# Optimization experiments

Measured on AMD Instinct MI355X. Metric: run time of the kernel, lower is better.

The kernel has to match this reference:

```python
import jax, jax.numpy as jnp
import numpy as np

N, D, E, L = 50000, 128, 800000, 3


def setup_inputs() -> dict:
    key = jax.random.key(0)
    ks = jax.random.split(key, 4)
    scale = 1.0 / np.sqrt(D)
    x = jax.random.normal(ks[0], (N, D), dtype=jnp.float32)
    edge_index = jax.random.randint(ks[1], (2, E), 0, N, dtype=jnp.int64)
    W1 = jax.random.normal(ks[2], (L, D, D), dtype=jnp.float32) * scale
    W2 = jax.random.normal(ks[3], (L, D, D), dtype=jnp.float32) * scale
    b1 = jnp.zeros((L, D), dtype=jnp.float32)
    b2 = jnp.zeros((L, D), dtype=jnp.float32)
    return {"x": x, "edge_index": edge_index, "W1": W1, "b1": b1, "W2": W2, "b2": b2}


def reference(x, edge_index, W1, b1, W2, b2):
    # GIN: for each conv, agg_i = (1+eps)*x_i + sum_{(j->i)} x_j  (eps=0),
    # then h = nn(agg) with nn = Linear->ReLU->Linear, then outer ReLU.
    src = edge_index[0]
    dst = edge_index[1]
    n = x.shape[0]
    for l in range(W1.shape[0]):
        agg = x + jax.ops.segment_sum(x[src], dst, num_segments=n)  # [N, D]
        h = jnp.maximum(agg @ W1[l] + b1[l], 0.0)                   # inner ReLU
        x = jnp.maximum(h @ W2[l] + b2[l], 0.0)                     # outer ReLU
    return x
```

## Files before the change

kernel.cpp:

```cpp
#include <hip/hip_runtime.h>
#include <cstdint>


constexpr int N = 50000;
constexpr int D = 128;
constexpr int E = 800000;
constexpr int L = 3;
constexpr int WROW = 136;
constexpr int PSH = 9;
constexpr int PN = 1 << PSH;
constexpr int K = (N + PN - 1) >> PSH;
constexpr int ABLK = 2048;
constexpr int NAB = (E + ABLK - 1) / ABLK;

typedef _Float16 f16;
typedef _Float16 f16x8 __attribute__((ext_vector_type(8)));
typedef float f32x4 __attribute__((ext_vector_type(4)));

__device__ __forceinline__ bool ei_is64(const int* ei) {
  return (ei[1] == 0) && (ei[3] == 0) && (ei[5] == 0);
}
__device__ __forceinline__ int ei_src(const int* ei, int e, bool is64) {
  return is64 ? ei[2 * (size_t)e] : ei[e];
}
__device__ __forceinline__ int ei_dst(const int* ei, int e, bool is64) {
  return is64 ? ei[2 * ((size_t)E + e)] : ei[(size_t)E + e];
}

__global__ __launch_bounds__(256) void k_init(const float* __restrict__ x0,
                                              const int* __restrict__ ei,
                                              const float* __restrict__ W1,
                                              const float* __restrict__ W2,
                                              f16* __restrict__ Wt,
                                              f16* __restrict__ xh,
                                              int2* __restrict__ srcdst,
                                              int* __restrict__ gcnt) {
  __shared__ int hist[K];
  const int bid = blockIdx.x;
  if (bid < 384) {
    int i = bid * 256 + threadIdx.x;
    int m = i >> 14;
    int c = (i >> 7) & 127;
    int k = i & 127;
    const float* src = (m < L) ? (W1 + (size_t)m * D * D)
                               : (W2 + (size_t)(m - L) * D * D);
    Wt[i] = (f16)src[(size_t)k * D + c];
  } else if (bid < 384 + 3125) {
    int i = (bid - 384) * 256 + threadIdx.x;
    float4 v0 = *(const float4*)(x0 + (size_t)i * 8);
    float4 v1 = *(const float4*)(x0 + (size_t)i * 8 + 4);
    f16x8 o = {(f16)v0.x, (f16)v0.y, (f16)v0.z, (f16)v0.w,
               (f16)v1.x, (f16)v1.y, (f16)v1.z, (f16)v1.w};
    *(f16x8*)(xh + (size_t)i * 8) = o;
  } else {
    const int b = bid - (384 + 3125);
    for (int i = threadIdx.x; i < K; i += 256) hist[i] = 0;
    __syncthreads();
    const int base = b * ABLK;
    const int nHere = min(ABLK, E - base);
    bool is64 = ei_is64(ei);
#pragma unroll
    for (int r = 0; r < ABLK / 256; ++r) {
      int idx = r * 256 + threadIdx.x;
      if (idx < nHere) {
        int e = base + idx;
        int s = ei_src(ei, e, is64);
        int d = ei_dst(ei, e, is64);
        srcdst[e] = make_int2(s, d);
        atomicAdd(&hist[d >> PSH], 1);
      }
    }
    __syncthreads();
    for (int i = threadIdx.x; i < K; i += 256) gcnt[i * NAB + b] = hist[i];
  }
}

__global__ __launch_bounds__(256) void k_gbase(const int* __restrict__ gcnt,
                                               int* __restrict__ gbase,
                                               int* __restrict__ psize) {
  __shared__ int s[256];
  __shared__ int carry;
  const int p = blockIdx.x;
  const int tid = threadIdx.x;
  if (tid == 0) carry = 0;
  __syncthreads();
  for (int chunk = 0; chunk < 2; ++chunk) {
    int i = chunk * 256 + tid;
    int v = (i < NAB) ? gcnt[p * NAB + i] : 0;
    s[tid] = v;
    __syncthreads();
#pragma unroll
    for (int o = 1; o < 256; o <<= 1) {
      int t = (tid >= o) ? s[tid - o] : 0;
      __syncthreads();
      s[tid] += t;
      __syncthreads();
    }
    int excl = s[tid] - v + carry;
    if (i < NAB) gbase[p * NAB + i] = excl;
    __syncthreads();
    if (tid == 255) carry = carry + s[255];
    __syncthreads();
  }
  if (tid == 0) psize[p] = carry;
}

__global__ __launch_bounds__(256) void k_pscan(const int* __restrict__ psize,
                                               int* __restrict__ pbase,
                                               int* __restrict__ off) {
  __shared__ int s[256];
  const int tid = threadIdx.x;
  int v = (tid < K) ? psize[tid] : 0;
  s[tid] = v;
  __syncthreads();
#pragma unroll
  for (int o = 1; o < 256; o <<= 1) {
    int t = (tid >= o) ? s[tid - o] : 0;
    __syncthreads();
    s[tid] += t;
    __syncthreads();
  }
  if (tid < K) pbase[tid] = s[tid] - v;
  if (tid == 0) { pbase[K] = E; off[N] = E; }
}

__global__ __launch_bounds__(256) void k_scat(const int2* __restrict__ srcdst,
                                              const int* __restrict__ gbase,
                                              const int* __restrict__ pbase,
                                              int2* __restrict__ part) {
  __shared__ int rankc[K];
  const int b = blockIdx.x;
  const int tid = threadIdx.x;
  for (int i = tid; i < K; i += 256) rankc[i] = 0;
  __syncthreads();
  const int base = b * ABLK;
  const int nHere = min(ABLK, E - base);
#pragma unroll
  for (int r = 0; r < ABLK / 256; ++r) {
    int idx = r * 256 + tid;
    if (idx < nHere) {
      int2 sd = srcdst[base + idx];
      int p = sd.y >> PSH;
      int lr = atomicAdd(&rankc[p], 1);
      part[pbase[p] + gbase[p * NAB + b] + lr] = sd;
    }
  }
}

__global__ __launch_bounds__(256) void k_fin(const int2* __restrict__ part,
                                             const int* __restrict__ pbase,
                                             int* __restrict__ off,
                                             int* __restrict__ ssrc) {
  __shared__ int hist[PN];
  __shared__ int bbase[PN];
  __shared__ int rc[PN];
  __shared__ int s[256];
  __shared__ int carry;
  const int p = blockIdx.x;
  const int tid = threadIdx.x;
  const int lo = p << PSH;
  const int nn = min(PN, N - lo);
  const int ebeg = pbase[p], eend = pbase[p + 1];
  for (int i = tid; i < PN; i += 256) { hist[i] = 0; rc[i] = 0; }
  if (tid == 0) carry = 0;
  __syncthreads();
  for (int e = ebeg + tid; e < eend; e += 256)
    atomicAdd(&hist[part[e].y - lo], 1);
  __syncthreads();
  for (int chunk = 0; chunk < PN / 256; ++chunk) {
    int i = chunk * 256 + tid;
    int v = hist[i];
    s[tid] = v;
    __syncthreads();
#pragma unroll
    for (int o = 1; o < 256; o <<= 1) {
      int t = (tid >= o) ? s[tid - o] : 0;
      __syncthreads();
      s[tid] += t;
      __syncthreads();
    }
    bbase[i] = s[tid] - v + carry;
    __syncthreads();
    if (tid == 255) carry = carry + s[255];
    __syncthreads();
  }
  for (int i = tid; i < nn; i += 256) off[lo + i] = ebeg + bbase[i];
  __syncthreads();
  for (int e = ebeg + tid; e < eend; e += 256) {
    int2 sd = part[e];
    int b = sd.y - lo;
    int r = atomicAdd(&rc[b], 1);
    ssrc[ebeg + bbase[b] + r] = sd.x;
  }
}

__global__ __launch_bounds__(256) void k_gather_f16(const f16* __restrict__ x,
                                                    const int* __restrict__ off,
                                                    const int* __restrict__ ssrc,
                                                    f16* __restrict__ agg) {
  int n = blockIdx.x * 16 + (threadIdx.x >> 4);
  if (n >= N) return;
  const int d0 = (threadIdx.x & 15) << 3;
  f16x8 v = *(const f16x8*)(x + (size_t)n * D + d0);
  float acc[8];
#pragma unroll
  for (int j = 0; j < 8; ++j) acc[j] = (float)v[j];
  const int beg = off[n], end = off[n + 1];
  int p = beg;
  for (; p + 8 <= end; p += 8) {
    f16x8 u[8];
#pragma unroll
    for (int q = 0; q < 8; ++q) {
      int s = ssrc[p + q];
      u[q] = *(const f16x8*)(x + (size_t)s * D + d0);
    }
#pragma unroll
    for (int q = 0; q < 8; ++q)
#pragma unroll
      for (int j = 0; j < 8; ++j) acc[j] += (float)u[q][j];
  }
  if (p + 4 <= end) {
    f16x8 u[4];
#pragma unroll
    for (int q = 0; q < 4; ++q) {
      int s = ssrc[p + q];
      u[q] = *(const f16x8*)(x + (size_t)s * D + d0);
    }
#pragma unroll
    for (int q = 0; q < 4; ++q)
#pragma unroll
      for (int j = 0; j < 8; ++j) acc[j] += (float)u[q][j];
    p += 4;
  }
  for (; p < end; ++p) {
    int s = ssrc[p];
    f16x8 u = *(const f16x8*)(x + (size_t)s * D + d0);
#pragma unroll
    for (int j = 0; j < 8; ++j) acc[j] += (float)u[j];
  }
  f16x8 o;
#pragma unroll
  for (int j = 0; j < 8; ++j) o[j] = (f16)acc[j];
  *(f16x8*)(agg + (size_t)n * D + d0) = o;
}

__global__ __launch_bounds__(256) void k_gemm_fused(const f16* __restrict__ A,
                                                    const f16* __restrict__ Wt1,
                                                    const f16* __restrict__ Wt2,
                                                    const float* __restrict__ b1,
                                                    const float* __restrict__ b2,
                                                    f16* __restrict__ Ch,
                                                    float* __restrict__ Cf) {
  __shared__ f16 Ws[2][128 * WROW];
  {
    const f16x8* g1 = (const f16x8*)Wt1;
    const f16x8* g2 = (const f16x8*)Wt2;
    for (int i = threadIdx.x; i < 2048; i += 256) {
      int c = i >> 4;
      int k8 = (i & 15) << 3;
      *(f16x8*)&Ws[0][c * WROW + k8] = g1[i];
      *(f16x8*)&Ws[1][c * WROW + k8] = g2[i];
    }
  }
  __syncthreads();

  const int w = threadIdx.x >> 6;
  const int l = threadIdx.x & 63;
  const int l15 = l & 15;
  const int g = l >> 4;
  const int r0 = blockIdx.x * 64 + w * 16;

  const int arow = min(r0 + l15, N - 1);
  const f16* Arow = A + (size_t)arow * D;
  f16x8 a[4];
#pragma unroll
  for (int t = 0; t < 4; ++t)
    a[t] = *(const f16x8*)(Arow + t * 32 + g * 8);

  float bc1[8], bc2[8];
#pragma unroll
  for (int c = 0; c < 8; ++c) {
    bc1[c] = b1[c * 16 + l15];
    bc2[c] = b2[c * 16 + l15];
  }

  f32x4 acc[8];
#pragma unroll
  for (int c = 0; c < 8; ++c) acc[c] = (f32x4){0.f, 0.f, 0.f, 0.f};
#pragma unroll
  for (int t = 0; t < 4; ++t) {
#pragma unroll
    for (int c = 0; c < 8; ++c) {
      f16x8 b = *(const f16x8*)&Ws[0][(c * 16 + l15) * WROW + t * 32 + g * 8];
      acc[c] = __builtin_amdgcn_mfma_f32_16x16x32_f16(a[t], b, acc[c], 0, 0, 0);
    }
  }

  __syncthreads();

  f16* hbuf = &Ws[0][0];
#pragma unroll
  for (int r = 0; r < 4; ++r) {
    int hr = w * 16 + g * 4 + r;
#pragma unroll
    for (int c = 0; c < 8; ++c) {
      float vv = fmaxf(acc[c][r] + bc1[c], 0.0f);
      hbuf[hr * WROW + c * 16 + l15] = (f16)vv;
    }
  }
  __syncthreads();

  f16x8 a2[4];
#pragma unroll
  for (int t = 0; t < 4; ++t)
    a2[t] = *(const f16x8*)&hbuf[(w * 16 + l15) * WROW + t * 32 + g * 8];

#pragma unroll
  for (int c = 0; c < 8; ++c) acc[c] = (f32x4){0.f, 0.f, 0.f, 0.f};
#pragma unroll
  for (int t = 0; t < 4; ++t) {
#pragma unroll
    for (int c = 0; c < 8; ++c) {
      f16x8 b = *(const f16x8*)&Ws[1][(c * 16 + l15) * WROW + t * 32 + g * 8];
      acc[c] = __builtin_amdgcn_mfma_f32_16x16x32_f16(a2[t], b, acc[c], 0, 0, 0);
    }
  }

#pragma unroll
  for (int r = 0; r < 4; ++r) {
    int rr = r0 + g * 4 + r;
    if (rr < N) {
#pragma unroll
      for (int c = 0; c < 8; ++c) {
        int col = c * 16 + l15;
        float vv = fmaxf(acc[c][r] + bc2[c], 0.0f);
        Ch[(size_t)rr * D + col] = (f16)vv;
        if (Cf) Cf[(size_t)rr * D + col] = vv;
      }
    }
  }
}

extern "C" void kernel_launch(void* const* d_in, const int* in_sizes, int n_in,
                              void* d_out, int out_size, void* d_ws, size_t ws_size,
                              hipStream_t stream) {
  const float* x0 = (const float*)d_in[0];
  const int* ei   = (const int*)d_in[1];
  const float* W1 = (const float*)d_in[2];
  const float* b1 = (const float*)d_in[3];
  const float* W2 = (const float*)d_in[4];
  const float* b2 = (const float*)d_in[5];
  float* out = (float*)d_out;

  f16* xh      = (f16*)d_ws;
  f16* aggh    = xh + (size_t)N * D;
  f16* Wt      = aggh + (size_t)N * D;
  int2* srcdst = (int2*)(Wt + (size_t)2 * L * D * D);
  int2* part   = srcdst + E;
  int* gcnt    = (int*)(part + E);
  int* gbase   = gcnt + (size_t)K * NAB;
  int* psize   = gbase + (size_t)K * NAB;
  int* pbase   = psize + K;
  int* off     = pbase + (K + 1);
  int* ssrc    = off + (N + 1);

  const dim3 blk(256);

  k_init<<<384 + 3125 + NAB, blk, 0, stream>>>(x0, ei, W1, W2, Wt, xh, srcdst,
                                               gcnt);
  k_gbase<<<K, blk, 0, stream>>>(gcnt, gbase, psize);
  k_pscan<<<1, blk, 0, stream>>>(psize, pbase, off);
  k_scat<<<NAB, blk, 0, stream>>>(srcdst, gbase, pbase, part);
  k_fin<<<K, blk, 0, stream>>>(part, pbase, off, ssrc);

  const int gemm_blocks = (N + 63) / 64;
  const int gather_blocks = N / 16;

  for (int l = 0; l < L; ++l) {
    k_gather_f16<<<gather_blocks, blk, 0, stream>>>(xh, off, ssrc, aggh);
    k_gemm_fused<<<gemm_blocks, blk, 0, stream>>>(
        aggh, Wt + (size_t)l * D * D, Wt + (size_t)(L + l) * D * D,
        b1 + (size_t)l * D, b2 + (size_t)l * D, xh,
        (l == L - 1) ? out : nullptr);
  }
}
```

Before: 193.4 us.

## Fuse neighbor gather and two-layer MLP into one per-layer kernel

Merges the gather kernel and the fused GEMM kernel into a single per-layer kernel. Each wave aggregates its own 16 rows into shared memory, then runs both MFMA GEMMs directly from that tile, with ping-pong node-feature buffers. Weight staging in shared memory is dropped; B fragments are read straight from global memory and cached. This removes the aggregate write and read-back plus one launch per layer and cuts LDS use. The cost is that each thread now walks four nodes' neighbor lists one after another, with far fewer threads in flight, so gather memory-level parallelism drops.

```diff
diff --git a/kernel.cpp b/kernel.cpp
--- a/kernel.cpp
+++ b/kernel.cpp
@@ -194,88 +194,78 @@
   }
 }
 
-__global__ __launch_bounds__(256) void k_gather_f16(const f16* __restrict__ x,
-                                                    const int* __restrict__ off,
-                                                    const int* __restrict__ ssrc,
-                                                    f16* __restrict__ agg) {
-  int n = blockIdx.x * 16 + (threadIdx.x >> 4);
-  if (n >= N) return;
-  const int d0 = (threadIdx.x & 15) << 3;
-  f16x8 v = *(const f16x8*)(x + (size_t)n * D + d0);
-  float acc[8];
-#pragma unroll
-  for (int j = 0; j < 8; ++j) acc[j] = (float)v[j];
-  const int beg = off[n], end = off[n + 1];
-  int p = beg;
-  for (; p + 8 <= end; p += 8) {
-    f16x8 u[8];
-#pragma unroll
-    for (int q = 0; q < 8; ++q) {
-      int s = ssrc[p + q];
-      u[q] = *(const f16x8*)(x + (size_t)s * D + d0);
-    }
-#pragma unroll
-    for (int q = 0; q < 8; ++q)
-#pragma unroll
-      for (int j = 0; j < 8; ++j) acc[j] += (float)u[q][j];
-  }
-  if (p + 4 <= end) {
-    f16x8 u[4];
-#pragma unroll
-    for (int q = 0; q < 4; ++q) {
-      int s = ssrc[p + q];
-      u[q] = *(const f16x8*)(x + (size_t)s * D + d0);
-    }
-#pragma unroll
-    for (int q = 0; q < 4; ++q)
-#pragma unroll
-      for (int j = 0; j < 8; ++j) acc[j] += (float)u[q][j];
-    p += 4;
-  }
-  for (; p < end; ++p) {
-    int s = ssrc[p];
-    f16x8 u = *(const f16x8*)(x + (size_t)s * D + d0);
-#pragma unroll
-    for (int j = 0; j < 8; ++j) acc[j] += (float)u[j];
-  }
-  f16x8 o;
-#pragma unroll
-  for (int j = 0; j < 8; ++j) o[j] = (f16)acc[j];
-  *(f16x8*)(agg + (size_t)n * D + d0) = o;
-}
-
-__global__ __launch_bounds__(256) void k_gemm_fused(const f16* __restrict__ A,
-                                                    const f16* __restrict__ Wt1,
-                                                    const f16* __restrict__ Wt2,
-                                                    const float* __restrict__ b1,
-                                                    const float* __restrict__ b2,
-                                                    f16* __restrict__ Ch,
-                                                    float* __restrict__ Cf) {
-  __shared__ f16 Ws[2][128 * WROW];
-  {
-    const f16x8* g1 = (const f16x8*)Wt1;
-    const f16x8* g2 = (const f16x8*)Wt2;
-    for (int i = threadIdx.x; i < 2048; i += 256) {
-      int c = i >> 4;
-      int k8 = (i & 15) << 3;
-      *(f16x8*)&Ws[0][c * WROW + k8] = g1[i];
-      *(f16x8*)&Ws[1][c * WROW + k8] = g2[i];
-    }
-  }
-  __syncthreads();
-
+__global__ __launch_bounds__(256) void k_layer(const f16* __restrict__ x,
+                                               const int* __restrict__ off,
+                                               const int* __restrict__ ssrc,
+                                               const f16* __restrict__ Wt1,
+                                               const f16* __restrict__ Wt2,
+                                               const float* __restrict__ b1,
+                                               const float* __restrict__ b2,
+                                               f16* __restrict__ Ch,
+                                               float* __restrict__ Cf) {
+  __shared__ f16 buf[64 * WROW];
   const int w = threadIdx.x >> 6;
   const int l = threadIdx.x & 63;
   const int l15 = l & 15;
-  const int g = l >> 4;
-  const int r0 = blockIdx.x * 64 + w * 16;
-
-  const int arow = min(r0 + l15, N - 1);
-  const f16* Arow = A + (size_t)arow * D;
+  const int gg = l >> 4;
+  const int base = blockIdx.x * 64;
+  const int d0 = l15 << 3;
+
+  for (int q = 0; q < 4; ++q) {
+    const int rb = w * 16 + gg * 4 + q;
+    const int n = base + rb;
+    f16x8 o;
+    if (n < N) {
+      f16x8 v = *(const f16x8*)(x + (size_t)n * D + d0);
+      float acc[8];
+#pragma unroll
+      for (int j = 0; j < 8; ++j) acc[j] = (float)v[j];
+      const int beg = off[n], end = off[n + 1];
+      int p = beg;
+      for (; p + 8 <= end; p += 8) {
+        f16x8 u[8];
+#pragma unroll
+        for (int t = 0; t < 8; ++t) {
+          int s = ssrc[p + t];
+          u[t] = *(const f16x8*)(x + (size_t)s * D + d0);
+        }
+#pragma unroll
+        for (int t = 0; t < 8; ++t)
+#pragma unroll
+          for (int j = 0; j < 8; ++j) acc[j] += (float)u[t][j];
+      }
+      if (p + 4 <= end) {
+        f16x8 u[4];
+#pragma unroll
+        for (int t = 0; t < 4; ++t) {
+          int s = ssrc[p + t];
+          u[t] = *(const f16x8*)(x + (size_t)s * D + d0);
+        }
+#pragma unroll
+        for (int t = 0; t < 4; ++t)
+#pragma unroll
+          for (int j = 0; j < 8; ++j) acc[j] += (float)u[t][j];
+        p += 4;
+      }
+      for (; p < end; ++p) {
+        int s = ssrc[p];
+        f16x8 u = *(const f16x8*)(x + (size_t)s * D + d0);
+#pragma unroll
+        for (int j = 0; j < 8; ++j) acc[j] += (float)u[j];
+      }
+#pragma unroll
+      for (int j = 0; j < 8; ++j) o[j] = (f16)acc[j];
+    } else {
+#pragma unroll
+      for (int j = 0; j < 8; ++j) o[j] = (f16)0.f;
+    }
+    *(f16x8*)&buf[rb * WROW + d0] = o;
+  }
+
   f16x8 a[4];
 #pragma unroll
   for (int t = 0; t < 4; ++t)
-    a[t] = *(const f16x8*)(Arow + t * 32 + g * 8);
+    a[t] = *(const f16x8*)&buf[(w * 16 + l15) * WROW + t * 32 + gg * 8];
 
   float bc1[8], bc2[8];
 #pragma unroll
@@ -291,29 +281,25 @@
   for (int t = 0; t < 4; ++t) {
 #pragma unroll
     for (int c = 0; c < 8; ++c) {
-      f16x8 b = *(const f16x8*)&Ws[0][(c * 16 + l15) * WROW + t * 32 + g * 8];
+      f16x8 b = *(const f16x8*)(Wt1 + ((c * 16 + l15) << 7) + t * 32 + (gg << 3));
       acc[c] = __builtin_amdgcn_mfma_f32_16x16x32_f16(a[t], b, acc[c], 0, 0, 0);
     }
   }
 
-  __syncthreads();
-
-  f16* hbuf = &Ws[0][0];
 #pragma unroll
   for (int r = 0; r < 4; ++r) {
-    int hr = w * 16 + g * 4 + r;
+    int hr = w * 16 + gg * 4 + r;
 #pragma unroll
     for (int c = 0; c < 8; ++c) {
       float vv = fmaxf(acc[c][r] + bc1[c], 0.0f);
-      hbuf[hr * WROW + c * 16 + l15] = (f16)vv;
-    }
-  }
-  __syncthreads();
+      buf[hr * WROW + c * 16 + l15] = (f16)vv;
+    }
+  }
 
   f16x8 a2[4];
 #pragma unroll
   for (int t = 0; t < 4; ++t)
-    a2[t] = *(const f16x8*)&hbuf[(w * 16 + l15) * WROW + t * 32 + g * 8];
+    a2[t] = *(const f16x8*)&buf[(w * 16 + l15) * WROW + t * 32 + gg * 8];
 
 #pragma unroll
   for (int c = 0; c < 8; ++c) acc[c] = (f32x4){0.f, 0.f, 0.f, 0.f};
@@ -321,14 +307,14 @@
   for (int t = 0; t < 4; ++t) {
 #pragma unroll
     for (int c = 0; c < 8; ++c) {
-      f16x8 b = *(const f16x8*)&Ws[1][(c * 16 + l15) * WROW + t * 32 + g * 8];
+      f16x8 b = *(const f16x8*)(Wt2 + ((c * 16 + l15) << 7) + t * 32 + (gg << 3));
       acc[c] = __builtin_amdgcn_mfma_f32_16x16x32_f16(a2[t], b, acc[c], 0, 0, 0);
     }
   }
 
 #pragma unroll
   for (int r = 0; r < 4; ++r) {
-    int rr = r0 + g * 4 + r;
+    int rr = base + w * 16 + gg * 4 + r;
     if (rr < N) {
 #pragma unroll
       for (int c = 0; c < 8; ++c) {
@@ -353,8 +339,8 @@
   float* out = (float*)d_out;
 
   f16* xh      = (f16*)d_ws;
-  f16* aggh    = xh + (size_t)N * D;
-  f16* Wt      = aggh + (size_t)N * D;
+  f16* xh2     = xh + (size_t)N * D;
+  f16* Wt      = xh2 + (size_t)N * D;
   int2* srcdst = (int2*)(Wt + (size_t)2 * L * D * D);
   int2* part   = srcdst + E;
   int* gcnt    = (int*)(part + E);
@@ -373,14 +359,15 @@
   k_scat<<<NAB, blk, 0, stream>>>(srcdst, gbase, pbase, part);
   k_fin<<<K, blk, 0, stream>>>(part, pbase, off, ssrc);
 
-  const int gemm_blocks = (N + 63) / 64;
-  const int gather_blocks = N / 16;
-
+  const int layer_blocks = (N + 63) / 64;
+
+  f16* cur = xh;
+  f16* nxt = xh2;
   for (int l = 0; l < L; ++l) {
-    k_gather_f16<<<gather_blocks, blk, 0, stream>>>(xh, off, ssrc, aggh);
-    k_gemm_fused<<<gemm_blocks, blk, 0, stream>>>(
-        aggh, Wt + (size_t)l * D * D, Wt + (size_t)(L + l) * D * D,
-        b1 + (size_t)l * D, b2 + (size_t)l * D, xh,
+    k_layer<<<layer_blocks, blk, 0, stream>>>(
+        cur, off, ssrc, Wt + (size_t)l * D * D, Wt + (size_t)(L + l) * D * D,
+        b1 + (size_t)l * D, b2 + (size_t)l * D, nxt,
         (l == L - 1) ? out : nullptr);
-  }
-}
+    f16* tmp = cur; cur = nxt; nxt = tmp;
+  }
+}
```

New measurement: 228.6 us. +18.2%, slower.
